# Kernel tuning notes

Hardware: AMD Instinct MI355X
Metric: run time of the kernel (lower is better)

Reference implementation:

```python
import jax, jax.numpy as jnp
import numpy as np

VNUM = 50000
OUT = 128
E = 1600000
EPS = 1e-7


def setup_inputs() -> dict:
    key = jax.random.key(0)
    k = jax.random.split(key, 8)
    sidx = jax.random.randint(k[0], (E,), 0, VNUM, dtype=jnp.int64 if jax.config.jax_enable_x64 else jnp.int32)
    tidx = jax.random.randint(k[1], (E,), 0, VNUM, dtype=sidx.dtype)
    enorm = jax.random.uniform(k[2], (E,), dtype=jnp.float32)
    # edge signs +-1 as in signed graph conv
    esgn = jnp.where(jax.random.uniform(k[3], (E,)) < 0.5, -1.0, 1.0).astype(jnp.float32)
    # vrepr initialized trunc_normal(std=0.1) (zero_init=False)
    vrepr = 0.1 * jax.random.truncated_normal(k[4], -2.0, 2.0, (VNUM, OUT), dtype=jnp.float32)
    lim = 1.0 / np.sqrt(OUT)
    loc_w = jax.random.uniform(k[5], (OUT, OUT), jnp.float32, -lim, lim)
    loc_b = jnp.zeros((OUT,), jnp.float32)
    std_w = jax.random.uniform(k[6], (OUT, OUT), jnp.float32, -lim, lim)
    std_b = jnp.zeros((OUT,), jnp.float32)
    return {"sidx": sidx, "tidx": tidx, "enorm": enorm, "esgn": esgn,
            "vrepr": vrepr, "loc_w": loc_w, "loc_b": loc_b,
            "std_w": std_w, "std_b": std_b}


def reference(sidx, tidx, enorm, esgn, vrepr, loc_w, loc_b, std_w, std_b):
    # GraphConv: edge-weighted gather + scatter-add aggregation
    msg = vrepr[sidx] * (esgn * enorm)[:, None]          # [E, OUT]
    ptr = jax.ops.segment_sum(msg, tidx, num_segments=VNUM)  # [VNUM, OUT]
    loc = ptr @ loc_w.T + loc_b                          # Normal loc
    std = jax.nn.softplus(ptr @ std_w.T + std_b) + EPS   # Normal scale
    return loc, std
```

## Files before the change

kernel.cpp:

```cpp
#include <hip/hip_runtime.h>
#include <math.h>

#define VNUM 50000
#define OUTF 128
#define NEDGE 1600000
#define EPSF 1e-7f

#define CONV_BLOCKS 6250
#define BFRAG_BLOCKS 64

#define CHUNK 2048
#define NCB 49
#define COARSE_BLOCKS 782
#define SUBS 8
#define NSB (NCB * SUBS)

typedef __attribute__((ext_vector_type(8))) short short8;
typedef __attribute__((ext_vector_type(4))) float v4f;

__device__ __forceinline__ unsigned short f2bf(float f) {
    union { float f; unsigned int u; } c; c.f = f;
    unsigned int u = c.u;
    return (unsigned short)((u + 0x7FFFu + ((u >> 16) & 1u)) >> 16);
}
__device__ __forceinline__ float bf16_lo(unsigned int p) {
    union { unsigned int u; float f; } c; c.u = p << 16; return c.f;
}
__device__ __forceinline__ float bf16_hi(unsigned int p) {
    union { unsigned int u; float f; } c; c.u = p & 0xFFFF0000u; return c.f;
}

__device__ __forceinline__ int wave_incl_scan(int v, int lane) {
#pragma unroll
    for (int off = 1; off < 64; off <<= 1) {
        const int o = __shfl_up(v, off, 64);
        if (lane >= off) v += o;
    }
    return v;
}

__global__ __launch_bounds__(256) void prep_kernel(
    const float* __restrict__ vrepr, unsigned int* __restrict__ vrepr16,
    const int* __restrict__ tidx, int* __restrict__ chist,
    const float* __restrict__ loc_w, const float* __restrict__ std_w,
    unsigned int* bfrag)
{
    __shared__ int lc[4][NCB];
    const int b = blockIdx.x, tid = threadIdx.x;
    if (b < CONV_BLOCKS) {
        const size_t base = (size_t)b * 1024 + tid * 4;
        const float4 v = *reinterpret_cast<const float4*>(vrepr + base);
        uint2 o;
        o.x = (unsigned)f2bf(v.x) | ((unsigned)f2bf(v.y) << 16);
        o.y = (unsigned)f2bf(v.z) | ((unsigned)f2bf(v.w) << 16);
        *reinterpret_cast<uint2*>(vrepr16 + base / 2) = o;
    } else if (b < CONV_BLOCKS + COARSE_BLOCKS) {
        const int hb = b - CONV_BLOCKS;
        for (int i = tid; i < 4 * NCB; i += 256) (&lc[0][0])[i] = 0;
        __syncthreads();
        const int base = hb * CHUNK;
#pragma unroll
        for (int j = 0; j < 8; ++j) {
            const int e = base + j * 256 + tid;
            if (e < NEDGE) atomicAdd(&lc[tid >> 6][tidx[e] >> 10], 1);
        }
        __syncthreads();
        if (tid < NCB) {
            const int s = lc[0][tid] + lc[1][tid] + lc[2][tid] + lc[3][tid];
            if (s) atomicAdd(&chist[tid], s);
        }
    } else {
        const int p = (b - (CONV_BLOCKS + COARSE_BLOCKS)) * 256 + tid;
        const int j2 = p & 3, lq = (p >> 2) & 63, ks = (p >> 8) & 3, ct = p >> 10;
        const int k = ks * 32 + (lq >> 4) * 8 + j2 * 2;
        const int n = ct * 16 + (lq & 15);
        const float* wsrc = (n >> 7) ? std_w : loc_w;
        const int c = n & 127;
        bfrag[p] = (unsigned)f2bf(wsrc[c * 128 + k]) |
                   ((unsigned)f2bf(wsrc[c * 128 + k + 1]) << 16);
    }
}

__global__ __launch_bounds__(64) void scan_coarse_kernel(
    const int* __restrict__ chist, int* __restrict__ cbase,
    int* __restrict__ ccursor, int* __restrict__ offs)
{
    const int tid = threadIdx.x;
    const int v = (tid < NCB) ? chist[tid] : 0;
    const int inc = wave_incl_scan(v, tid);
    const int ex = inc - v;
    if (tid < NCB) { cbase[tid] = ex; ccursor[tid] = ex; }
    if (tid == NCB - 1) { cbase[NCB] = inc; offs[VNUM] = inc; }
}

__global__ __launch_bounds__(256) void coarse_kernel(
    const int* __restrict__ sidx, const int* __restrict__ tidx,
    const float* __restrict__ enorm, const float* __restrict__ esgn,
    int* __restrict__ ccursor, uint2* __restrict__ coarse8)
{
    __shared__ uint2 lrec[CHUNK];
    __shared__ int lcnt[4][NCB];
    __shared__ int lbase[4][NCB];
    __shared__ int loffs[NCB];
    __shared__ int grun[NCB];

    const int tid = threadIdx.x, lane = tid & 63, wv = tid >> 6;
    const int base = blockIdx.x * CHUNK;
    const int n = min(CHUNK, NEDGE - base);

    for (int i = tid; i < 4 * NCB; i += 256) (&lcnt[0][0])[i] = 0;
    __syncthreads();

    uint2 rec[8];
#pragma unroll
    for (int j = 0; j < 8; ++j) {
        const int e = base + j * 256 + tid;
        if (e < NEDGE) {
            const int t = tidx[e];
            const float w = esgn[e] * enorm[e];
            rec[j].x = ((unsigned)sidx[e] << 16) | (unsigned)f2bf(w);
            rec[j].y = (unsigned)t;
            atomicAdd(&lcnt[wv][t >> 10], 1);
        }
    }
    __syncthreads();

    if (tid < 64) {
        int c0 = 0, c1 = 0, c2 = 0, c3 = 0, tot = 0;
        if (lane < NCB) {
            c0 = lcnt[0][lane]; c1 = lcnt[1][lane];
            c2 = lcnt[2][lane]; c3 = lcnt[3][lane];
            tot = c0 + c1 + c2 + c3;
        }
        const int inc = wave_incl_scan(tot, lane);
        const int ex = inc - tot;
        if (lane < NCB) {
            loffs[lane]    = ex;
            lbase[0][lane] = ex;
            lbase[1][lane] = ex + c0;
            lbase[2][lane] = ex + c0 + c1;
            lbase[3][lane] = ex + c0 + c1 + c2;
            grun[lane] = atomicAdd(&ccursor[lane], tot);
        }
    }
    __syncthreads();

#pragma unroll
    for (int j = 0; j < 8; ++j) {
        const int e = base + j * 256 + tid;
        if (e < NEDGE) {
            const int cb = (int)(rec[j].y >> 10);
            const int pos = atomicAdd(&lbase[wv][cb], 1);
            lrec[pos] = rec[j];
        }
    }
    __syncthreads();

    for (int i = tid; i < n; i += 256) {
        const uint2 r = lrec[i];
        const int cb = (int)(r.y >> 10);
        coarse8[grun[cb] + (i - loffs[cb])] = r;
    }
}

__global__ __launch_bounds__(256) void binhist_kernel(
    const uint2* __restrict__ coarse8, const int* __restrict__ cbase,
    int* __restrict__ bcnt)
{
    __shared__ int lc[1024];
    const int tid = threadIdx.x;
    const int bin = blockIdx.x >> 3, sub = blockIdx.x & (SUBS - 1);
    for (int i = tid; i < 1024; i += 256) lc[i] = 0;
    __syncthreads();
    const int s0 = cbase[bin];
    const int L  = cbase[bin + 1] - s0;
    const int beg = s0 + (L * sub) / SUBS;
    const int end = s0 + (L * (sub + 1)) / SUBS;
    for (int i = beg + tid; i < end; i += 256)
        atomicAdd(&lc[coarse8[i].y & 1023], 1);
    __syncthreads();
    for (int i = tid; i < 1024; i += 256)
        bcnt[(blockIdx.x << 10) + i] = lc[i];
}

__global__ __launch_bounds__(256) void scan_bin_kernel(
    const int* __restrict__ bcnt, const int* __restrict__ cbase,
    int* __restrict__ offs, int* __restrict__ fcur)
{
    __shared__ int wsum[4];
    const int tid = threadIdx.x, lane = tid & 63, wv = tid >> 6;
    const int bin = blockIdx.x;
    const int i0 = tid * 4;

    int c[SUBS][4];
#pragma unroll
    for (int s = 0; s < SUBS; ++s) {
        const int base = ((bin * SUBS + s) << 10) + i0;
#pragma unroll
        for (int j = 0; j < 4; ++j) c[s][j] = bcnt[base + j];
    }
    int tot[4];
#pragma unroll
    for (int j = 0; j < 4; ++j) {
        int t2 = 0;
#pragma unroll
        for (int s = 0; s < SUBS; ++s) t2 += c[s][j];
        tot[j] = t2;
    }
    const int ts = tot[0] + tot[1] + tot[2] + tot[3];
    const int inc = wave_incl_scan(ts, lane);
    if (lane == 63) wsum[wv] = inc;
    __syncthreads();
    int run = cbase[bin] + (inc - ts);
    for (int w2 = 0; w2 < wv; ++w2) run += wsum[w2];

#pragma unroll
    for (int j = 0; j < 4; ++j) {
        const int v = (bin << 10) + i0 + j;
        if (v < VNUM) offs[v] = run;
        int p = run;
#pragma unroll
        for (int s = 0; s < SUBS; ++s) {
            fcur[((bin * SUBS + s) << 10) + i0 + j] = p;
            p += c[s][j];
        }
        run += tot[j];
    }
}

__global__ __launch_bounds__(256) void fine_kernel(
    const uint2* __restrict__ coarse8, const int* __restrict__ cbase,
    const int* __restrict__ fcur, unsigned int* __restrict__ pairs)
{
    __shared__ int lfc[1024];
    const int tid = threadIdx.x;
    const int bin = blockIdx.x >> 3, sub = blockIdx.x & (SUBS - 1);
    for (int i = tid; i < 1024; i += 256)
        lfc[i] = fcur[(blockIdx.x << 10) + i];
    __syncthreads();
    const int s0 = cbase[bin];
    const int L  = cbase[bin + 1] - s0;
    const int beg = s0 + (L * sub) / SUBS;
    const int end = s0 + (L * (sub + 1)) / SUBS;
    for (int i = beg + tid; i < end; i += 256) {
        const uint2 r = coarse8[i];
        const int pos = atomicAdd(&lfc[r.y & 1023], 1);
        pairs[pos] = r.x;
    }
}

__global__ __launch_bounds__(256) void aggregate_kernel(
    const int* __restrict__ offs, const unsigned int* __restrict__ pairs,
    const unsigned int* __restrict__ vrepr16, float* __restrict__ acc)
{
    const int v = blockIdx.x * 4 + (threadIdx.x >> 6);
    const int l = threadIdx.x & 63;
    int i = offs[v];
    const int end = offs[v + 1];

    float a0 = 0.0f, a1 = 0.0f;
    for (; i + 4 <= end; i += 4) {
        const unsigned p0 = pairs[i], p1 = pairs[i + 1];
        const unsigned p2 = pairs[i + 2], p3 = pairs[i + 3];
        const unsigned r0 = vrepr16[(size_t)(p0 >> 16) * 64 + l];
        const unsigned r1 = vrepr16[(size_t)(p1 >> 16) * 64 + l];
        const unsigned r2 = vrepr16[(size_t)(p2 >> 16) * 64 + l];
        const unsigned r3 = vrepr16[(size_t)(p3 >> 16) * 64 + l];
        const float w0 = bf16_lo(p0), w1 = bf16_lo(p1);
        const float w2 = bf16_lo(p2), w3 = bf16_lo(p3);
        a0 = fmaf(bf16_lo(r0), w0, a0); a1 = fmaf(bf16_hi(r0), w0, a1);
        a0 = fmaf(bf16_lo(r1), w1, a0); a1 = fmaf(bf16_hi(r1), w1, a1);
        a0 = fmaf(bf16_lo(r2), w2, a0); a1 = fmaf(bf16_hi(r2), w2, a1);
        a0 = fmaf(bf16_lo(r3), w3, a0); a1 = fmaf(bf16_hi(r3), w3, a1);
    }
    for (; i < end; ++i) {
        const unsigned p = pairs[i];
        const unsigned r = vrepr16[(size_t)(p >> 16) * 64 + l];
        const float w = bf16_lo(p);
        a0 = fmaf(bf16_lo(r), w, a0); a1 = fmaf(bf16_hi(r), w, a1);
    }
    *reinterpret_cast<float2*>(acc + (size_t)v * OUTF + 2 * l) = make_float2(a0, a1);
}

__global__ __launch_bounds__(256) void gemm_mfma_kernel(
    const float* acc, const unsigned int* __restrict__ bfrag,
    const float* __restrict__ loc_b, const float* __restrict__ std_b,
    float* out)
{
    __shared__ unsigned short tile[16][136];
    const int t = threadIdx.x;
    const int row0 = blockIdx.x * 16;
    const int l = t & 63, w = t >> 6;

    short8 bfr[4][4];
#pragma unroll
    for (int ct = 0; ct < 4; ++ct)
#pragma unroll
        for (int ks = 0; ks < 4; ++ks)
            bfr[ct][ks] = *reinterpret_cast<const short8*>(
                bfrag + ((((w * 4 + ct) * 4 + ks) * 64 + l) << 2));

    {
        const float* src = acc + (size_t)row0 * OUTF + t * 8;
        const float4 v0 = *reinterpret_cast<const float4*>(src);
        const float4 v1 = *reinterpret_cast<const float4*>(src + 4);
        uint4 pk;
        pk.x = (unsigned)f2bf(v0.x) | ((unsigned)f2bf(v0.y) << 16);
        pk.y = (unsigned)f2bf(v0.z) | ((unsigned)f2bf(v0.w) << 16);
        pk.z = (unsigned)f2bf(v1.x) | ((unsigned)f2bf(v1.y) << 16);
        pk.w = (unsigned)f2bf(v1.z) | ((unsigned)f2bf(v1.w) << 16);
        *reinterpret_cast<uint4*>(&tile[t >> 4][(t & 15) * 8]) = pk;
    }
    __syncthreads();

    const int m = l & 15, q = l >> 4;
    v4f accv[4];
#pragma unroll
    for (int ct = 0; ct < 4; ++ct) accv[ct] = (v4f){0.0f, 0.0f, 0.0f, 0.0f};

#pragma unroll
    for (int ks = 0; ks < 4; ++ks) {
        const short8 a = *reinterpret_cast<const short8*>(&tile[m][ks * 32 + q * 8]);
#pragma unroll
        for (int ct = 0; ct < 4; ++ct)
            accv[ct] = __builtin_amdgcn_mfma_f32_16x16x32_bf16(
                a, bfr[ct][ks], accv[ct], 0, 0, 0);
    }

#pragma unroll
    for (int ct = 0; ct < 4; ++ct) {
        const int colg = (w * 4 + ct) * 16 + m;
        const int h = colg >> 7, c = colg & 127;
        const float bias = (h ? std_b : loc_b)[c];
        float* dst = out + (h ? (size_t)VNUM * OUTF : (size_t)0);
#pragma unroll
        for (int reg = 0; reg < 4; ++reg) {
            const int row = row0 + q * 4 + reg;
            float x = accv[ct][reg] + bias;
            if (h) x = fmaxf(x, 0.0f) + log1pf(expf(-fabsf(x))) + EPSF;
            dst[(size_t)row * OUTF + c] = x;
        }
    }
}

__global__ __launch_bounds__(256) void gemm_fallback_kernel(
    const float* acc,
    const float* __restrict__ loc_w, const float* __restrict__ loc_b,
    const float* __restrict__ std_w, const float* __restrict__ std_b,
    float* out)
{
    __shared__ float tile[16][OUTF];
    const int t = threadIdx.x;
    const int row0 = blockIdx.x * 16;
    {
        const float4* src = reinterpret_cast<const float4*>(acc + (size_t)row0 * OUTF);
        float4* dst = reinterpret_cast<float4*>(&tile[0][0]);
        dst[t] = src[t]; dst[t + 256] = src[t + 256];
    }
    __syncthreads();
    const int is_std = t >> 7;
    const int c = t & 127;
    const float* w = (is_std ? std_w : loc_w) + (size_t)c * OUTF;
    const float bias = is_std ? std_b[c] : loc_b[c];
    float accv[16];
#pragma unroll
    for (int r = 0; r < 16; ++r) accv[r] = 0.0f;
    for (int k = 0; k < OUTF; k += 4) {
        const float4 wv = *reinterpret_cast<const float4*>(w + k);
#pragma unroll
        for (int r = 0; r < 16; ++r) {
            const float4 pv = *reinterpret_cast<const float4*>(&tile[r][k]);
            float a = accv[r];
            a = fmaf(pv.x, wv.x, a); a = fmaf(pv.y, wv.y, a);
            a = fmaf(pv.z, wv.z, a); a = fmaf(pv.w, wv.w, a);
            accv[r] = a;
        }
    }
    float* dst_base = out + (is_std ? (size_t)VNUM * OUTF : (size_t)0);
#pragma unroll
    for (int r = 0; r < 16; ++r) {
        const float x = accv[r] + bias;
        dst_base[(size_t)(row0 + r) * OUTF + c] =
            is_std ? (fmaxf(x, 0.0f) + log1pf(expf(-fabsf(x))) + EPSF) : x;
    }
}

extern "C" void kernel_launch(void* const* d_in, const int* in_sizes, int n_in,
                              void* d_out, int out_size, void* d_ws, size_t ws_size,
                              hipStream_t stream) {
    const int*   sidx  = (const int*)  d_in[0];
    const int*   tidx  = (const int*)  d_in[1];
    const float* enorm = (const float*)d_in[2];
    const float* esgn  = (const float*)d_in[3];
    const float* vrepr = (const float*)d_in[4];
    const float* loc_w = (const float*)d_in[5];
    const float* loc_b = (const float*)d_in[6];
    const float* std_w = (const float*)d_in[7];
    const float* std_b = (const float*)d_in[8];

    float* out = (float*)d_out;
    float* acc = out;

    uint2* coarse8 = (uint2*)out;

    unsigned int* sbase   = (unsigned int*)(out + (size_t)VNUM * OUTF);
    unsigned int* pairs   = sbase;
    unsigned int* vrepr16 = sbase + NEDGE;
    int* bcnt    = (int*)(sbase + NEDGE + (size_t)VNUM * 64);
    int* fcur    = bcnt + NSB * 1024;
    int* offs    = fcur + NSB * 1024;
    int* cbase   = offs + VNUM + 1;
    int* ccursor = cbase + NCB + 1;
    int* chist   = ccursor + NCB;

    const bool use_ws = ws_size >= 16384 * sizeof(unsigned int);
    unsigned int* bfrag = use_ws ? (unsigned int*)d_ws : nullptr;

    hipMemsetAsync(chist, 0, NCB * sizeof(int), stream);

    const int prep_blocks = CONV_BLOCKS + COARSE_BLOCKS + (use_ws ? BFRAG_BLOCKS : 0);
    prep_kernel       <<<prep_blocks, 256, 0, stream>>>(vrepr, vrepr16, tidx, chist,
                                                        loc_w, std_w, bfrag);
    scan_coarse_kernel<<<1, 64, 0, stream>>>(chist, cbase, ccursor, offs);
    coarse_kernel     <<<COARSE_BLOCKS, 256, 0, stream>>>(sidx, tidx, enorm, esgn,
                                                          ccursor, coarse8);
    binhist_kernel    <<<NSB, 256, 0, stream>>>(coarse8, cbase, bcnt);
    scan_bin_kernel   <<<NCB, 256, 0, stream>>>(bcnt, cbase, offs, fcur);
    fine_kernel       <<<NSB, 256, 0, stream>>>(coarse8, cbase, fcur, pairs);
    aggregate_kernel  <<<VNUM / 4, 256, 0, stream>>>(offs, pairs, vrepr16, acc);

    if (use_ws) {
        gemm_mfma_kernel<<<VNUM / 16, 256, 0, stream>>>(acc, bfrag, loc_b, std_b, out);
    } else {
        gemm_fallback_kernel<<<VNUM / 16, 256, 0, stream>>>(acc, loc_w, loc_b,
                                                            std_w, std_b, out);
    }
}
```

Before: 270.9 us.

## Fuse bin sort into one kernel and fuse aggregation with MFMA GEMM

Replaces the three-kernel fine sort (histogram, scan, scatter across 8 sub-blocks per bin) with a single 1024-thread block per coarse bin that counts, scans and scatters in shared memory. When the workspace is large enough, gather-aggregation and the bf16 MFMA projection are fused into one kernel that keeps the 16-row aggregate tile in LDS, avoiding the fp32 accumulator round trip through global memory. The fused bin sort uses only 49 blocks, which may underuse the GPU, and the old non-workspace fallback GEMM is removed.

Result: slower. 304.4 us (+12.4%).

```diff
diff --git a/kernel.cpp b/kernel.cpp
--- a/kernel.cpp
+++ b/kernel.cpp
@@ -12,8 +12,6 @@
 #define CHUNK 2048
 #define NCB 49
 #define COARSE_BLOCKS 782
-#define SUBS 8
-#define NSB (NCB * SUBS)
 
 typedef __attribute__((ext_vector_type(8))) short short8;
 typedef __attribute__((ext_vector_type(4))) float v4f;
@@ -163,89 +161,122 @@
     }
 }
 
-__global__ __launch_bounds__(256) void binhist_kernel(
+__global__ __launch_bounds__(1024) void binsort_kernel(
     const uint2* __restrict__ coarse8, const int* __restrict__ cbase,
-    int* __restrict__ bcnt)
-{
-    __shared__ int lc[1024];
-    const int tid = threadIdx.x;
-    const int bin = blockIdx.x >> 3, sub = blockIdx.x & (SUBS - 1);
-    for (int i = tid; i < 1024; i += 256) lc[i] = 0;
-    __syncthreads();
-    const int s0 = cbase[bin];
-    const int L  = cbase[bin + 1] - s0;
-    const int beg = s0 + (L * sub) / SUBS;
-    const int end = s0 + (L * (sub + 1)) / SUBS;
-    for (int i = beg + tid; i < end; i += 256)
-        atomicAdd(&lc[coarse8[i].y & 1023], 1);
-    __syncthreads();
-    for (int i = tid; i < 1024; i += 256)
-        bcnt[(blockIdx.x << 10) + i] = lc[i];
-}
-
-__global__ __launch_bounds__(256) void scan_bin_kernel(
-    const int* __restrict__ bcnt, const int* __restrict__ cbase,
-    int* __restrict__ offs, int* __restrict__ fcur)
-{
-    __shared__ int wsum[4];
+    int* __restrict__ offs, unsigned int* __restrict__ pairs)
+{
+    __shared__ int cnt[1024];
+    __shared__ int cur[1024];
+    __shared__ int wsum[16];
     const int tid = threadIdx.x, lane = tid & 63, wv = tid >> 6;
     const int bin = blockIdx.x;
-    const int i0 = tid * 4;
-
-    int c[SUBS][4];
-#pragma unroll
-    for (int s = 0; s < SUBS; ++s) {
-        const int base = ((bin * SUBS + s) << 10) + i0;
-#pragma unroll
-        for (int j = 0; j < 4; ++j) c[s][j] = bcnt[base + j];
-    }
-    int tot[4];
-#pragma unroll
-    for (int j = 0; j < 4; ++j) {
-        int t2 = 0;
-#pragma unroll
-        for (int s = 0; s < SUBS; ++s) t2 += c[s][j];
-        tot[j] = t2;
-    }
-    const int ts = tot[0] + tot[1] + tot[2] + tot[3];
-    const int inc = wave_incl_scan(ts, lane);
+    const int s0 = cbase[bin], e0 = cbase[bin + 1];
+
+    cnt[tid] = 0;
+    __syncthreads();
+    for (int i = s0 + tid; i < e0; i += 1024)
+        atomicAdd(&cnt[coarse8[i].y & 1023], 1);
+    __syncthreads();
+
+    const int v = cnt[tid];
+    const int inc = wave_incl_scan(v, lane);
     if (lane == 63) wsum[wv] = inc;
     __syncthreads();
-    int run = cbase[bin] + (inc - ts);
-    for (int w2 = 0; w2 < wv; ++w2) run += wsum[w2];
-
-#pragma unroll
-    for (int j = 0; j < 4; ++j) {
-        const int v = (bin << 10) + i0 + j;
-        if (v < VNUM) offs[v] = run;
-        int p = run;
-#pragma unroll
-        for (int s = 0; s < SUBS; ++s) {
-            fcur[((bin * SUBS + s) << 10) + i0 + j] = p;
-            p += c[s][j];
-        }
-        run += tot[j];
-    }
-}
-
-__global__ __launch_bounds__(256) void fine_kernel(
-    const uint2* __restrict__ coarse8, const int* __restrict__ cbase,
-    const int* __restrict__ fcur, unsigned int* __restrict__ pairs)
-{
-    __shared__ int lfc[1024];
-    const int tid = threadIdx.x;
-    const int bin = blockIdx.x >> 3, sub = blockIdx.x & (SUBS - 1);
-    for (int i = tid; i < 1024; i += 256)
-        lfc[i] = fcur[(blockIdx.x << 10) + i];
-    __syncthreads();
-    const int s0 = cbase[bin];
-    const int L  = cbase[bin + 1] - s0;
-    const int beg = s0 + (L * sub) / SUBS;
-    const int end = s0 + (L * (sub + 1)) / SUBS;
-    for (int i = beg + tid; i < end; i += 256) {
+    if (tid == 0) {
+        int run = 0;
+        for (int i2 = 0; i2 < 16; ++i2) { const int t2 = wsum[i2]; wsum[i2] = run; run += t2; }
+    }
+    __syncthreads();
+    const int ex = s0 + wsum[wv] + inc - v;
+    const int gv = (bin << 10) + tid;
+    if (gv < VNUM) offs[gv] = ex;
+    cur[tid] = ex;
+    __syncthreads();
+
+    for (int i = s0 + tid; i < e0; i += 1024) {
         const uint2 r = coarse8[i];
-        const int pos = atomicAdd(&lfc[r.y & 1023], 1);
+        const int pos = atomicAdd(&cur[r.y & 1023], 1);
         pairs[pos] = r.x;
+    }
+}
+
+__global__ __launch_bounds__(256) void aggemm_kernel(
+    const int* __restrict__ offs, const unsigned int* __restrict__ pairs,
+    const unsigned int* __restrict__ vrepr16,
+    const unsigned int* __restrict__ bfrag,
+    const float* __restrict__ loc_b, const float* __restrict__ std_b,
+    float* out)
+{
+    __shared__ unsigned short tile[16][136];
+    const int t = threadIdx.x, l = t & 63, w = t >> 6;
+    const int row0 = blockIdx.x * 16;
+
+#pragma unroll
+    for (int r = 0; r < 4; ++r) {
+        const int vtx = row0 + w * 4 + r;
+        int i = offs[vtx];
+        const int end = offs[vtx + 1];
+        float a0 = 0.0f, a1 = 0.0f;
+        for (; i + 4 <= end; i += 4) {
+            const unsigned p0 = pairs[i], p1 = pairs[i + 1];
+            const unsigned p2 = pairs[i + 2], p3 = pairs[i + 3];
+            const unsigned r0 = vrepr16[(size_t)(p0 >> 16) * 64 + l];
+            const unsigned r1 = vrepr16[(size_t)(p1 >> 16) * 64 + l];
+            const unsigned r2 = vrepr16[(size_t)(p2 >> 16) * 64 + l];
+            const unsigned r3 = vrepr16[(size_t)(p3 >> 16) * 64 + l];
+            const float w0 = bf16_lo(p0), w1 = bf16_lo(p1);
+            const float w2 = bf16_lo(p2), w3 = bf16_lo(p3);
+            a0 = fmaf(bf16_lo(r0), w0, a0); a1 = fmaf(bf16_hi(r0), w0, a1);
+            a0 = fmaf(bf16_lo(r1), w1, a0); a1 = fmaf(bf16_hi(r1), w1, a1);
+            a0 = fmaf(bf16_lo(r2), w2, a0); a1 = fmaf(bf16_hi(r2), w2, a1);
+            a0 = fmaf(bf16_lo(r3), w3, a0); a1 = fmaf(bf16_hi(r3), w3, a1);
+        }
+        for (; i < end; ++i) {
+            const unsigned p = pairs[i];
+            const unsigned rr = vrepr16[(size_t)(p >> 16) * 64 + l];
+            const float ww = bf16_lo(p);
+            a0 = fmaf(bf16_lo(rr), ww, a0); a1 = fmaf(bf16_hi(rr), ww, a1);
+        }
+        const unsigned pk = (unsigned)f2bf(a0) | ((unsigned)f2bf(a1) << 16);
+        *reinterpret_cast<unsigned*>(&tile[w * 4 + r][2 * l]) = pk;
+    }
+
+    short8 bfr[4][4];
+#pragma unroll
+    for (int ct = 0; ct < 4; ++ct)
+#pragma unroll
+        for (int ks = 0; ks < 4; ++ks)
+            bfr[ct][ks] = *reinterpret_cast<const short8*>(
+                bfrag + ((((w * 4 + ct) * 4 + ks) * 64 + l) << 2));
+    __syncthreads();
+
+    const int m = l & 15, q = l >> 4;
+    v4f accv[4];
+#pragma unroll
+    for (int ct = 0; ct < 4; ++ct) accv[ct] = (v4f){0.0f, 0.0f, 0.0f, 0.0f};
+
+#pragma unroll
+    for (int ks = 0; ks < 4; ++ks) {
+        const short8 a = *reinterpret_cast<const short8*>(&tile[m][ks * 32 + q * 8]);
+#pragma unroll
+        for (int ct = 0; ct < 4; ++ct)
+            accv[ct] = __builtin_amdgcn_mfma_f32_16x16x32_bf16(
+                a, bfr[ct][ks], accv[ct], 0, 0, 0);
+    }
+
+#pragma unroll
+    for (int ct = 0; ct < 4; ++ct) {
+        const int colg = (w * 4 + ct) * 16 + m;
+        const int h = colg >> 7, c = colg & 127;
+        const float bias = (h ? std_b : loc_b)[c];
+        float* dst = out + (h ? (size_t)VNUM * OUTF : (size_t)0);
+#pragma unroll
+        for (int reg = 0; reg < 4; ++reg) {
+            const int row = row0 + q * 4 + reg;
+            float x = accv[ct][reg] + bias;
+            if (h) x = fmaxf(x, 0.0f) + log1pf(expf(-fabsf(x))) + EPSF;
+            dst[(size_t)row * OUTF + c] = x;
+        }
     }
 }
 
@@ -343,48 +374,6 @@
     }
 }
 
-__global__ __launch_bounds__(256) void gemm_fallback_kernel(
-    const float* acc,
-    const float* __restrict__ loc_w, const float* __restrict__ loc_b,
-    const float* __restrict__ std_w, const float* __restrict__ std_b,
-    float* out)
-{
-    __shared__ float tile[16][OUTF];
-    const int t = threadIdx.x;
-    const int row0 = blockIdx.x * 16;
-    {
-        const float4* src = reinterpret_cast<const float4*>(acc + (size_t)row0 * OUTF);
-        float4* dst = reinterpret_cast<float4*>(&tile[0][0]);
-        dst[t] = src[t]; dst[t + 256] = src[t + 256];
-    }
-    __syncthreads();
-    const int is_std = t >> 7;
-    const int c = t & 127;
-    const float* w = (is_std ? std_w : loc_w) + (size_t)c * OUTF;
-    const float bias = is_std ? std_b[c] : loc_b[c];
-    float accv[16];
-#pragma unroll
-    for (int r = 0; r < 16; ++r) accv[r] = 0.0f;
-    for (int k = 0; k < OUTF; k += 4) {
-        const float4 wv = *reinterpret_cast<const float4*>(w + k);
-#pragma unroll
-        for (int r = 0; r < 16; ++r) {
-            const float4 pv = *reinterpret_cast<const float4*>(&tile[r][k]);
-            float a = accv[r];
-            a = fmaf(pv.x, wv.x, a); a = fmaf(pv.y, wv.y, a);
-            a = fmaf(pv.z, wv.z, a); a = fmaf(pv.w, wv.w, a);
-            accv[r] = a;
-        }
-    }
-    float* dst_base = out + (is_std ? (size_t)VNUM * OUTF : (size_t)0);
-#pragma unroll
-    for (int r = 0; r < 16; ++r) {
-        const float x = accv[r] + bias;
-        dst_base[(size_t)(row0 + r) * OUTF + c] =
-            is_std ? (fmaxf(x, 0.0f) + log1pf(expf(-fabsf(x))) + EPSF) : x;
-    }
-}
-
 extern "C" void kernel_launch(void* const* d_in, const int* in_sizes, int n_in,
                               void* d_out, int out_size, void* d_ws, size_t ws_size,
                               hipStream_t stream) {
@@ -399,40 +388,54 @@
     const float* std_b = (const float*)d_in[8];
 
     float* out = (float*)d_out;
-    float* acc = out;
 
     uint2* coarse8 = (uint2*)out;
 
-    unsigned int* sbase   = (unsigned int*)(out + (size_t)VNUM * OUTF);
-    unsigned int* pairs   = sbase;
-    unsigned int* vrepr16 = sbase + NEDGE;
-    int* bcnt    = (int*)(sbase + NEDGE + (size_t)VNUM * 64);
-    int* fcur    = bcnt + NSB * 1024;
-    int* offs    = fcur + NSB * 1024;
-    int* cbase   = offs + VNUM + 1;
-    int* ccursor = cbase + NCB + 1;
-    int* chist   = ccursor + NCB;
-
-    const bool use_ws = ws_size >= 16384 * sizeof(unsigned int);
-    unsigned int* bfrag = use_ws ? (unsigned int*)d_ws : nullptr;
+    unsigned int* sbase = (unsigned int*)(out + (size_t)VNUM * OUTF);
+    const size_t WS_WORDS_NEED = 16384 + (VNUM + 1) + NEDGE + (size_t)VNUM * 64;
+    const bool fused = ws_size >= WS_WORDS_NEED * sizeof(unsigned int);
+
+    unsigned int* bfrag;
+    int* offs;
+    unsigned int* pairs;
+    unsigned int* vrepr16;
+    int *cbase, *ccursor, *chist;
+
+    if (fused) {
+        unsigned int* wsb = (unsigned int*)d_ws;
+        bfrag   = wsb;
+        offs    = (int*)(wsb + 16384);
+        pairs   = wsb + 16384 + (VNUM + 1);
+        vrepr16 = pairs + NEDGE;
+        cbase   = (int*)sbase;
+        ccursor = cbase + NCB + 1;
+        chist   = ccursor + NCB;
+    } else {
+        pairs   = sbase;
+        vrepr16 = sbase + NEDGE;
+        offs    = (int*)(sbase + NEDGE + (size_t)VNUM * 64);
+        cbase   = offs + VNUM + 1;
+        ccursor = cbase + NCB + 1;
+        chist   = ccursor + NCB;
+        bfrag   = (unsigned int*)d_ws;
+    }
 
     hipMemsetAsync(chist, 0, NCB * sizeof(int), stream);
 
-    const int prep_blocks = CONV_BLOCKS + COARSE_BLOCKS + (use_ws ? BFRAG_BLOCKS : 0);
+    const int prep_blocks = CONV_BLOCKS + COARSE_BLOCKS + BFRAG_BLOCKS;
     prep_kernel       <<<prep_blocks, 256, 0, stream>>>(vrepr, vrepr16, tidx, chist,
                                                         loc_w, std_w, bfrag);
     scan_coarse_kernel<<<1, 64, 0, stream>>>(chist, cbase, ccursor, offs);
     coarse_kernel     <<<COARSE_BLOCKS, 256, 0, stream>>>(sidx, tidx, enorm, esgn,
                                                           ccursor, coarse8);
-    binhist_kernel    <<<NSB, 256, 0, stream>>>(coarse8, cbase, bcnt);
-    scan_bin_kernel   <<<NCB, 256, 0, stream>>>(bcnt, cbase, offs, fcur);
-    fine_kernel       <<<NSB, 256, 0, stream>>>(coarse8, cbase, fcur, pairs);
-    aggregate_kernel  <<<VNUM / 4, 256, 0, stream>>>(offs, pairs, vrepr16, acc);
-
-    if (use_ws) {
+    binsort_kernel    <<<NCB, 1024, 0, stream>>>(coarse8, cbase, offs, pairs);
+
+    if (fused) {
+        aggemm_kernel<<<VNUM / 16, 256, 0, stream>>>(offs, pairs, vrepr16, bfrag,
+                                                     loc_b, std_b, out);
+    } else {
+        float* acc = out;
+        aggregate_kernel<<<VNUM / 4, 256, 0, stream>>>(offs, pairs, vrepr16, acc);
         gemm_mfma_kernel<<<VNUM / 16, 256, 0, stream>>>(acc, bfrag, loc_b, std_b, out);
-    } else {
-        gemm_fallback_kernel<<<VNUM / 16, 256, 0, stream>>>(acc, loc_w, loc_b,
-                                                            std_w, std_b, out);
-    }
-}
+    }
+}
```

## Fuse fine-bin histogram, scan and scatter into one per-bin kernel; unroll aggregate by 8

Applied to the files above, without the earlier changes.

Replaces the three-kernel fine sort (sub-block histogram, scan, scatter) with a single binsort kernel per coarse bin. It uses 1024 threads that build the 1024-entry histogram in LDS, scan it and scatter pairs. This removes two launches and the global bcnt/fcur traffic. The catch is that only 49 blocks run, each reading about 32K records twice, which leaves most CUs idle on a large GPU. The aggregate loop also gains an 8-wide unrolled gather to raise memory-level parallelism.

Result: no change. 266.7 us (-1.5%).

```diff
diff --git a/kernel.cpp b/kernel.cpp
--- a/kernel.cpp
+++ b/kernel.cpp
@@ -12,8 +12,6 @@
 #define CHUNK 2048
 #define NCB 49
 #define COARSE_BLOCKS 782
-#define SUBS 8
-#define NSB (NCB * SUBS)
 
 typedef __attribute__((ext_vector_type(8))) short short8;
 typedef __attribute__((ext_vector_type(4))) float v4f;
@@ -163,88 +161,41 @@
     }
 }
 
-__global__ __launch_bounds__(256) void binhist_kernel(
+__global__ __launch_bounds__(1024) void binsort_kernel(
     const uint2* __restrict__ coarse8, const int* __restrict__ cbase,
-    int* __restrict__ bcnt)
-{
-    __shared__ int lc[1024];
-    const int tid = threadIdx.x;
-    const int bin = blockIdx.x >> 3, sub = blockIdx.x & (SUBS - 1);
-    for (int i = tid; i < 1024; i += 256) lc[i] = 0;
-    __syncthreads();
-    const int s0 = cbase[bin];
-    const int L  = cbase[bin + 1] - s0;
-    const int beg = s0 + (L * sub) / SUBS;
-    const int end = s0 + (L * (sub + 1)) / SUBS;
-    for (int i = beg + tid; i < end; i += 256)
-        atomicAdd(&lc[coarse8[i].y & 1023], 1);
-    __syncthreads();
-    for (int i = tid; i < 1024; i += 256)
-        bcnt[(blockIdx.x << 10) + i] = lc[i];
-}
-
-__global__ __launch_bounds__(256) void scan_bin_kernel(
-    const int* __restrict__ bcnt, const int* __restrict__ cbase,
-    int* __restrict__ offs, int* __restrict__ fcur)
-{
-    __shared__ int wsum[4];
+    int* __restrict__ offs, unsigned int* __restrict__ pairs)
+{
+    __shared__ int cnt[1024];
+    __shared__ int cur[1024];
+    __shared__ int wsum[16];
     const int tid = threadIdx.x, lane = tid & 63, wv = tid >> 6;
     const int bin = blockIdx.x;
-    const int i0 = tid * 4;
-
-    int c[SUBS][4];
-#pragma unroll
-    for (int s = 0; s < SUBS; ++s) {
-        const int base = ((bin * SUBS + s) << 10) + i0;
-#pragma unroll
-        for (int j = 0; j < 4; ++j) c[s][j] = bcnt[base + j];
-    }
-    int tot[4];
-#pragma unroll
-    for (int j = 0; j < 4; ++j) {
-        int t2 = 0;
-#pragma unroll
-        for (int s = 0; s < SUBS; ++s) t2 += c[s][j];
-        tot[j] = t2;
-    }
-    const int ts = tot[0] + tot[1] + tot[2] + tot[3];
-    const int inc = wave_incl_scan(ts, lane);
+    const int s0 = cbase[bin], e0 = cbase[bin + 1];
+
+    cnt[tid] = 0;
+    __syncthreads();
+    for (int i = s0 + tid; i < e0; i += 1024)
+        atomicAdd(&cnt[coarse8[i].y & 1023], 1);
+    __syncthreads();
+
+    const int v = cnt[tid];
+    const int inc = wave_incl_scan(v, lane);
     if (lane == 63) wsum[wv] = inc;
     __syncthreads();
-    int run = cbase[bin] + (inc - ts);
-    for (int w2 = 0; w2 < wv; ++w2) run += wsum[w2];
-
-#pragma unroll
-    for (int j = 0; j < 4; ++j) {
-        const int v = (bin << 10) + i0 + j;
-        if (v < VNUM) offs[v] = run;
-        int p = run;
-#pragma unroll
-        for (int s = 0; s < SUBS; ++s) {
-            fcur[((bin * SUBS + s) << 10) + i0 + j] = p;
-            p += c[s][j];
-        }
-        run += tot[j];
-    }
-}
-
-__global__ __launch_bounds__(256) void fine_kernel(
-    const uint2* __restrict__ coarse8, const int* __restrict__ cbase,
-    const int* __restrict__ fcur, unsigned int* __restrict__ pairs)
-{
-    __shared__ int lfc[1024];
-    const int tid = threadIdx.x;
-    const int bin = blockIdx.x >> 3, sub = blockIdx.x & (SUBS - 1);
-    for (int i = tid; i < 1024; i += 256)
-        lfc[i] = fcur[(blockIdx.x << 10) + i];
-    __syncthreads();
-    const int s0 = cbase[bin];
-    const int L  = cbase[bin + 1] - s0;
-    const int beg = s0 + (L * sub) / SUBS;
-    const int end = s0 + (L * (sub + 1)) / SUBS;
-    for (int i = beg + tid; i < end; i += 256) {
+    if (tid == 0) {
+        int run = 0;
+        for (int i2 = 0; i2 < 16; ++i2) { const int t2 = wsum[i2]; wsum[i2] = run; run += t2; }
+    }
+    __syncthreads();
+    const int ex = s0 + wsum[wv] + inc - v;
+    const int gv = (bin << 10) + tid;
+    if (gv < VNUM) offs[gv] = ex;
+    cur[tid] = ex;
+    __syncthreads();
+
+    for (int i = s0 + tid; i < e0; i += 1024) {
         const uint2 r = coarse8[i];
-        const int pos = atomicAdd(&lfc[r.y & 1023], 1);
+        const int pos = atomicAdd(&cur[r.y & 1023], 1);
         pairs[pos] = r.x;
     }
 }
@@ -259,6 +210,19 @@
     const int end = offs[v + 1];
 
     float a0 = 0.0f, a1 = 0.0f;
+    for (; i + 8 <= end; i += 8) {
+        unsigned p[8], r[8];
+#pragma unroll
+        for (int j = 0; j < 8; ++j) p[j] = pairs[i + j];
+#pragma unroll
+        for (int j = 0; j < 8; ++j) r[j] = vrepr16[(size_t)(p[j] >> 16) * 64 + l];
+#pragma unroll
+        for (int j = 0; j < 8; ++j) {
+            const float w = bf16_lo(p[j]);
+            a0 = fmaf(bf16_lo(r[j]), w, a0);
+            a1 = fmaf(bf16_hi(r[j]), w, a1);
+        }
+    }
     for (; i + 4 <= end; i += 4) {
         const unsigned p0 = pairs[i], p1 = pairs[i + 1];
         const unsigned p2 = pairs[i + 2], p3 = pairs[i + 3];
@@ -399,16 +363,13 @@
     const float* std_b = (const float*)d_in[8];
 
     float* out = (float*)d_out;
-    float* acc = out;
 
     uint2* coarse8 = (uint2*)out;
 
     unsigned int* sbase   = (unsigned int*)(out + (size_t)VNUM * OUTF);
     unsigned int* pairs   = sbase;
     unsigned int* vrepr16 = sbase + NEDGE;
-    int* bcnt    = (int*)(sbase + NEDGE + (size_t)VNUM * 64);
-    int* fcur    = bcnt + NSB * 1024;
-    int* offs    = fcur + NSB * 1024;
+    int* offs    = (int*)(sbase + NEDGE + (size_t)VNUM * 64);
     int* cbase   = offs + VNUM + 1;
     int* ccursor = cbase + NCB + 1;
     int* chist   = ccursor + NCB;
@@ -424,10 +385,10 @@
     scan_coarse_kernel<<<1, 64, 0, stream>>>(chist, cbase, ccursor, offs);
     coarse_kernel     <<<COARSE_BLOCKS, 256, 0, stream>>>(sidx, tidx, enorm, esgn,
                                                           ccursor, coarse8);
-    binhist_kernel    <<<NSB, 256, 0, stream>>>(coarse8, cbase, bcnt);
-    scan_bin_kernel   <<<NCB, 256, 0, stream>>>(bcnt, cbase, offs, fcur);
-    fine_kernel       <<<NSB, 256, 0, stream>>>(coarse8, cbase, fcur, pairs);
-    aggregate_kernel  <<<VNUM / 4, 256, 0, stream>>>(offs, pairs, vrepr16, acc);
+    binsort_kernel    <<<NCB, 1024, 0, stream>>>(coarse8, cbase, offs, pairs);
+
+    float* acc = out;
+    aggregate_kernel<<<VNUM / 4, 256, 0, stream>>>(offs, pairs, vrepr16, acc);
 
     if (use_ws) {
         gemm_mfma_kernel<<<VNUM / 16, 256, 0, stream>>>(acc, bfrag, loc_b, std_b, out);
```
